# Optimization experiments

Measured on AMD Instinct MI355X. Metric: run time of the kernel, lower is better.

Reference implementation:

```python
import jax, jax.numpy as jnp
import numpy as np

B, N, K = 8, 2048, 16   # batch, points, neighbors (after dropping self)
EPS = 1e-5


def _bn(y, g, b, m, v):
    # eval-mode batchnorm over channel dim 1, y: [B,C,...]
    sh = (1, -1) + (1,) * (y.ndim - 2)
    inv = g.reshape(sh) / jnp.sqrt(v.reshape(sh) + EPS)
    return (y - m.reshape(sh)) * inv + b.reshape(sh)


def setup_inputs() -> dict:
    key = jax.random.key(0)
    ks = jax.random.split(key, 16)
    d = {}
    d["x"] = jax.random.normal(ks[0], (B, 3, N), dtype=jnp.float32)
    # pre: Conv1d(3->24, k=1) + BN
    d["w_pre"] = jax.random.normal(ks[1], (24, 3), dtype=jnp.float32) * 0.3
    d["b_pre"] = jax.random.normal(ks[2], (24,), dtype=jnp.float32) * 0.1
    d["g_pre"] = 1.0 + 0.1 * jax.random.normal(ks[3], (24,), dtype=jnp.float32)
    d["be_pre"] = 0.1 * jax.random.normal(ks[4], (24,), dtype=jnp.float32)
    d["m_pre"] = 0.1 * jax.random.normal(ks[5], (24,), dtype=jnp.float32)
    d["v_pre"] = jax.random.uniform(ks[6], (24,), minval=0.5, maxval=1.5, dtype=jnp.float32)
    # shared_mlp_1: Conv2d(48->12, 1, bias=False) + BN
    d["w1"] = jax.random.normal(ks[7], (12, 48), dtype=jnp.float32) * 0.15
    d["g1"] = 1.0 + 0.1 * jax.random.normal(ks[8], (12,), dtype=jnp.float32)
    d["be1"] = 0.1 * jax.random.normal(ks[9], (12,), dtype=jnp.float32)
    d["m1"] = 0.1 * jax.random.normal(ks[10], (12,), dtype=jnp.float32)
    d["v1"] = jax.random.uniform(ks[11], (12,), minval=0.5, maxval=1.5, dtype=jnp.float32)
    # shared_mlp_2: Conv2d(60->12, 1, bias=False) + BN
    d["w2"] = jax.random.normal(ks[12], (12, 60), dtype=jnp.float32) * 0.15
    d["g2"] = 1.0 + 0.1 * jax.random.normal(ks[13], (12,), dtype=jnp.float32)
    d["be2"] = 0.1 * jax.random.normal(ks[14], (12,), dtype=jnp.float32)
    d["m2"] = 0.1 * jax.random.normal(ks[15], (12,), dtype=jnp.float32)
    d["v2"] = jnp.ones((12,), dtype=jnp.float32)
    # shared_mlp_3: Conv2d(72->12, 1, bias=False), no BN
    d["w3"] = jax.random.normal(jax.random.fold_in(key, 99), (12, 72), dtype=jnp.float32) * 0.15
    return d


def reference(x, w_pre, b_pre, g_pre, be_pre, m_pre, v_pre,
              w1, g1, be1, m1, v1, w2, g2, be2, m2, v2, w3):
    # pre: 1x1 conv1d + BN + ReLU -> [B,24,N]
    pre = jnp.einsum('oc,bcn->bon', w_pre, x) + b_pre[None, :, None]
    pre = jax.nn.relu(_bn(pre, g_pre, be_pre, m_pre, v_pre))

    # kNN on xyz = x.detach(): [B,N,3]
    pts = jax.lax.stop_gradient(jnp.swapaxes(x, 1, 2))
    sq = jnp.sum(pts * pts, axis=-1)                              # [B,N]
    d2 = sq[:, :, None] + sq[:, None, :] - 2.0 * jnp.einsum('bnc,bmc->bnm', pts, pts)
    _, idx = jax.lax.top_k(-d2, K + 1)                             # nearest K+1 incl. self
    idx = idx[..., 1:]                                             # drop self -> [B,N,K]

    # gather neighbor features: [B,24,N,K]
    grouped = jax.vmap(lambda f, i: f[:, i])(pre, idx)
    center = jnp.broadcast_to(pre[..., None], grouped.shape)
    y = jnp.concatenate([center, grouped], axis=1)                 # [B,48,N,K]

    h1 = jax.nn.relu(_bn(jnp.einsum('oc,bcnk->bonk', w1, y), g1, be1, m1, v1))
    y = jnp.concatenate([h1, y], axis=1)                           # [B,60,N,K]
    h2 = jax.nn.relu(_bn(jnp.einsum('oc,bcnk->bonk', w2, y), g2, be2, m2, v2))
    y = jnp.concatenate([h2, y], axis=1)                           # [B,72,N,K]
    h3 = jnp.einsum('oc,bcnk->bonk', w3, y)
    y = jnp.concatenate([h3, y], axis=1)                           # [B,84,N,K]

    y = jnp.max(y, axis=-1)                                        # maxpool over neighbors -> [B,84,N]
    return jnp.concatenate([y, x], axis=1)                         # [B,87,N]
```

## Files before the change

kernel.cpp:

```cpp
#include <hip/hip_runtime.h>
#include <math.h>

#define EPS 1e-5f
#define NBATCH 8
#define NPTS 2048
#define KNB 16
#define BIG 3.2e38f

#define KNN_BLKS (NBATCH * 64)
#define FUSED_LDS 54400

#define WS_PRE 0
#define WS_AUX (16384 * 24)
#define WS_IDX (WS_AUX + 16384 * 72)

__device__ __forceinline__ float dist2f(float mex, float mey, float mez,
                                        float sqn, float4 q) {
  float dot2 = fmaf(mex, q.x, fmaf(mey, q.y, __fmul_rn(mez, q.z)));
  return __fsub_rn(__fadd_rn(sqn, q.w), dot2);
}

__global__ __launch_bounds__(512, 4) void fused_kernel(
    const float* __restrict__ x,
    const float* __restrict__ w_pre, const float* __restrict__ b_pre,
    const float* __restrict__ g_pre, const float* __restrict__ be_pre,
    const float* __restrict__ m_pre, const float* __restrict__ v_pre,
    const float* __restrict__ w1, const float* __restrict__ g1,
    const float* __restrict__ be1, const float* __restrict__ m1,
    const float* __restrict__ v1,
    const float* __restrict__ w2, const float* __restrict__ g2,
    const float* __restrict__ be2, const float* __restrict__ m2,
    const float* __restrict__ v2, const float* __restrict__ w3,
    float* __restrict__ pre, float* __restrict__ aux,
    int* __restrict__ knn_out) {
  extern __shared__ char smem[];
  float4* C4   = (float4*)smem;
  float* slist = (float*)(smem + 32768);
  float* fwp = (float*)(smem + 32768);
  float* fbp = fwp + 72;
  float* fw1 = fbp + 24;
  float* fb1 = fw1 + 576;
  float* fw2 = fb1 + 12;
  float* fb2 = fw2 + 720;
  float* sd2   = (float*)(smem + 49152);
  int*   sidx  = (int*)(smem + 51712);
  int*   scnt  = (int*)(smem + 54272);

  int tid = threadIdx.x;
  int bi = blockIdx.x;
  int b = bi >> 6, chunk = bi & 63;
  const float* xb = x + (size_t)b * 3 * NPTS;

  for (int j = tid; j < NPTS; j += 512) {
    float xx = xb[j], yy = xb[NPTS + j], zz = xb[2 * NPTS + j];
    float sq = __fadd_rn(__fadd_rn(__fmul_rn(xx, xx), __fmul_rn(yy, yy)),
                         __fmul_rn(zz, zz));
    C4[j] = make_float4(2.0f * xx, 2.0f * yy, 2.0f * zz, sq);
  }
  if (tid < 72) { int o = tid / 3; fwp[tid] = w_pre[tid] * (g_pre[o] / sqrtf(v_pre[o] + EPS)); }
  if (tid < 24) { float inv = g_pre[tid] / sqrtf(v_pre[tid] + EPS);
                  fbp[tid] = (b_pre[tid] - m_pre[tid]) * inv + be_pre[tid]; }
  for (int j = tid; j < 576; j += 512) { int o = j / 48; fw1[j] = w1[j] * (g1[o] / sqrtf(v1[o] + EPS)); }
  if (tid < 12) { float inv = g1[tid] / sqrtf(v1[tid] + EPS); fb1[tid] = be1[tid] - m1[tid] * inv; }
  for (int j = tid; j < 720; j += 512) { int o = j / 60; fw2[j] = w2[j] * (g2[o] / sqrtf(v2[o] + EPS)); }
  if (tid < 12) { float inv = g2[tid] / sqrtf(v2[tid] + EPS); fb2[tid] = be2[tid] - m2[tid] * inv; }
  for (int j = tid; j < 32 * 20; j += 512) sidx[j] = 0;
  if (tid < 32) scnt[tid] = 0;
  __syncthreads();

  {
    int r = tid & 15, pt = tid >> 4;
    int n0 = chunk * 32 + pt;
    size_t pgl = (size_t)(b << 11) + n0;
    float x0 = xb[n0], x1 = xb[NPTS + n0], x2 = xb[2 * NPTS + n0];
    float pr[24];
#pragma unroll
    for (int c = 0; c < 24; ++c) {
      float v = fmaf(fwp[c * 3 + 0], x0,
                fmaf(fwp[c * 3 + 1], x1,
                fmaf(fwp[c * 3 + 2], x2, fbp[c])));
      pr[c] = fmaxf(v, 0.f);
    }
    if (r == 0) {
      float4* o4 = (float4*)(pre + pgl * 24);
#pragma unroll
      for (int i = 0; i < 6; ++i)
        o4[i] = make_float4(pr[4*i], pr[4*i+1], pr[4*i+2], pr[4*i+3]);
    }
    if (r < 12) {
      int o = r;
      float u1 = fb1[o], a1 = 0.f, u2 = fb2[o], a2 = 0.f, u3 = 0.f, a3 = 0.f;
#pragma unroll
      for (int i = 0; i < 24; ++i) {
        u1 = fmaf(fw1[o*48 + i],      pr[i], u1);
        a1 = fmaf(fw1[o*48 + 24 + i], pr[i], a1);
        u2 = fmaf(fw2[o*60 + 12 + i], pr[i], u2);
        a2 = fmaf(fw2[o*60 + 36 + i], pr[i], a2);
        u3 = fmaf(w3[o*72 + 24 + i],  pr[i], u3);
        a3 = fmaf(w3[o*72 + 48 + i],  pr[i], a3);
      }
      float* A = aux + pgl * 72;
      A[o] = u1; A[12 + o] = u2; A[24 + o] = u3;
      A[36 + o] = a1; A[48 + o] = a2; A[60 + o] = a3;
    }
  }
  __syncthreads();

  int p = tid & 31, s = tid >> 5;
  int n = chunk * 32 + p;
  float4 me4 = C4[n];
  float mex = 0.5f * me4.x, mey = 0.5f * me4.y, mez = 0.5f * me4.z;
  float sqn = me4.w;
  const float4* Cs = C4 + s * 128;
  int selfc = n - s * 128;
  float L[16];
#pragma unroll
  for (int t = 0; t < 16; ++t) L[t] = BIG;
  for (int c0 = 0; c0 < 128; c0 += 16) {
    float S[16];
#pragma unroll
    for (int cc = 0; cc < 16; ++cc) {
      float4 q = Cs[c0 + cc];
      float d2 = dist2f(mex, mey, mez, sqn, q);
      S[cc] = ((c0 + cc) == selfc) ? BIG : d2;
    }
#pragma unroll
    for (int pw = 1; pw < 16; pw <<= 1) {
#pragma unroll
      for (int k = pw; k >= 1; k >>= 1) {
#pragma unroll
        for (int j = (k & (pw - 1)); j + k < 16; j += 2 * k) {
#pragma unroll
          for (int i = 0; i < k; ++i) {
            int a = i + j, bq = i + j + k;
            if (bq < 16 && (a / (2 * pw) == bq / (2 * pw))) {
              float lo = fminf(S[a], S[bq]);
              float hi = fmaxf(S[a], S[bq]);
              S[a] = lo; S[bq] = hi;
            }
          }
        }
      }
    }
    float m[16];
#pragma unroll
    for (int i = 0; i < 16; ++i) m[i] = fminf(L[i], S[15 - i]);
#pragma unroll
    for (int d = 8; d >= 1; d >>= 1) {
#pragma unroll
      for (int i = 0; i < 16; ++i) {
        if (!(i & d)) {
          float lo = fminf(m[i], m[i | d]);
          float hi = fmaxf(m[i], m[i | d]);
          m[i] = lo; m[i | d] = hi;
        }
      }
    }
#pragma unroll
    for (int i = 0; i < 16; ++i) L[i] = m[i];
  }
  {
    float bb[16], m16[16];
#pragma unroll
    for (int i = 0; i < 16; ++i) bb[i] = __shfl_xor(L[i], 32, 64);
#pragma unroll
    for (int i = 0; i < 16; ++i) m16[i] = fminf(L[i], bb[15 - i]);
#pragma unroll
    for (int d = 8; d >= 1; d >>= 1) {
#pragma unroll
      for (int i = 0; i < 16; ++i) {
        if (!(i & d)) {
          float lo = fminf(m16[i], m16[i | d]);
          float hi = fmaxf(m16[i], m16[i | d]);
          m16[i] = lo; m16[i | d] = hi;
        }
      }
    }
    if (!(s & 1)) {
#pragma unroll
      for (int i = 0; i < 16; ++i) slist[((s >> 1) * 16 + i) * 32 + p] = m16[i];
    }
  }
  __syncthreads();
  for (int W = 4; W >= 1; W >>= 1) {
    int w = tid >> 5;
    bool act = (w < W);
    float a[16], bb[16];
    if (act) {
#pragma unroll
      for (int i = 0; i < 16; ++i) a[i]  = slist[((2 * w) * 16 + i) * 32 + p];
#pragma unroll
      for (int i = 0; i < 16; ++i) bb[i] = slist[((2 * w + 1) * 16 + i) * 32 + p];
    }
    __syncthreads();
    if (act) {
      float m16[16];
#pragma unroll
      for (int i = 0; i < 16; ++i) m16[i] = fminf(a[i], bb[15 - i]);
#pragma unroll
      for (int d = 8; d >= 1; d >>= 1) {
#pragma unroll
        for (int i = 0; i < 16; ++i) {
          if (!(i & d)) {
            float lo = fminf(m16[i], m16[i | d]);
            float hi = fmaxf(m16[i], m16[i | d]);
            m16[i] = lo; m16[i | d] = hi;
          }
        }
      }
#pragma unroll
      for (int i = 0; i < 16; ++i) slist[(w * 16 + i) * 32 + p] = m16[i];
    }
    __syncthreads();
  }
  float tau = slist[15 * 32 + p];
#pragma unroll 4
  for (int c = 0; c < 128; ++c) {
    float4 q = Cs[c];
    float d2 = dist2f(mex, mey, mez, sqn, q);
    int j = s * 128 + c;
    if (d2 <= tau && j != n) {
      int pos = atomicAdd(&scnt[p], 1);
      if (pos < 20) { sd2[p * 20 + pos] = d2; sidx[p * 20 + pos] = j; }
    }
  }
  __syncthreads();
  if (tid < 32) {
    int c = scnt[tid]; if (c > 20) c = 20;
    if (c > 16) {
      for (int t = 0; t < 16; ++t) {
        int best = t;
        for (int u = t + 1; u < c; ++u) {
          float da = sd2[tid * 20 + u], db = sd2[tid * 20 + best];
          int ia = sidx[tid * 20 + u], ib = sidx[tid * 20 + best];
          if (da < db || (da == db && ia < ib)) best = u;
        }
        float td = sd2[tid * 20 + t]; sd2[tid * 20 + t] = sd2[tid * 20 + best]; sd2[tid * 20 + best] = td;
        int ti = sidx[tid * 20 + t]; sidx[tid * 20 + t] = sidx[tid * 20 + best]; sidx[tid * 20 + best] = ti;
      }
    }
  }
  __syncthreads();
  {
    int pp = tid >> 4, kk = tid & 15;
    knn_out[((size_t)b * NPTS + chunk * 32 + pp) * KNB + kk] = sidx[pp * 20 + kk];
  }
}

__global__ __launch_bounds__(256) void mlp_kernel(
    const float* __restrict__ pre, const float* __restrict__ aux,
    const int* __restrict__ knn, const float* __restrict__ x,
    const float* __restrict__ w2, const float* __restrict__ g2,
    const float* __restrict__ v2, const float* __restrict__ w3,
    float* __restrict__ out) {
  __shared__ float sW2h[144], sW3h2[144], sW3h1[144];
  __shared__ float sout[87 * 16];
  int tid = threadIdx.x;
  if (tid < 144) {
    int o = tid / 12, i = tid - o * 12;
    float inv2 = g2[o] / sqrtf(v2[o] + EPS);
    sW2h[tid]  = w2[o * 60 + i] * inv2;
    sW3h2[tid] = w3[o * 72 + i];
    sW3h1[tid] = w3[o * 72 + 12 + i];
  }
  __syncthreads();
  int k = tid & 15, pl = tid >> 4;
  int p = blockIdx.x * 16 + pl;
  int b = p >> 11, n = p & (NPTS - 1);
  int nb = knn[(size_t)p * KNB + k];
  const float4* u4 = (const float4*)(aux + (size_t)p * 72);
  const float4* a4 = (const float4*)(aux + ((size_t)(b << 11) + nb) * 72 + 36);
  float uc[36], av[36];
#pragma unroll
  for (int i = 0; i < 9; ++i) {
    float4 t = u4[i];
    uc[4*i] = t.x; uc[4*i+1] = t.y; uc[4*i+2] = t.z; uc[4*i+3] = t.w;
    float4 t2 = a4[i];
    av[4*i] = t2.x; av[4*i+1] = t2.y; av[4*i+2] = t2.z; av[4*i+3] = t2.w;
  }
  float h1[12], h2[12], h3[12];
#pragma unroll
  for (int o = 0; o < 12; ++o) h1[o] = fmaxf(uc[o] + av[o], 0.f);
#pragma unroll
  for (int o = 0; o < 12; ++o) {
    float a = uc[12 + o] + av[12 + o];
#pragma unroll
    for (int i = 0; i < 12; ++i) a = fmaf(sW2h[o * 12 + i], h1[i], a);
    h2[o] = fmaxf(a, 0.f);
  }
#pragma unroll
  for (int o = 0; o < 12; ++o) {
    float a = uc[24 + o] + av[24 + o];
#pragma unroll
    for (int i = 0; i < 12; ++i) a = fmaf(sW3h2[o * 12 + i], h2[i], a);
#pragma unroll
    for (int i = 0; i < 12; ++i) a = fmaf(sW3h1[o * 12 + i], h1[i], a);
    h3[o] = a;
  }
  float nbf[24];
  const float4* pn4 = (const float4*)(pre + ((size_t)(b << 11) + nb) * 24);
#pragma unroll
  for (int i = 0; i < 6; ++i) {
    float4 t = pn4[i];
    nbf[4*i] = t.x; nbf[4*i+1] = t.y; nbf[4*i+2] = t.z; nbf[4*i+3] = t.w;
  }
#pragma unroll
  for (int m = 1; m < 16; m <<= 1) {
#pragma unroll
    for (int o = 0; o < 12; ++o) {
      h1[o] = fmaxf(h1[o], __shfl_xor(h1[o], m, 16));
      h2[o] = fmaxf(h2[o], __shfl_xor(h2[o], m, 16));
      h3[o] = fmaxf(h3[o], __shfl_xor(h3[o], m, 16));
    }
#pragma unroll
    for (int i = 0; i < 24; ++i)
      nbf[i] = fmaxf(nbf[i], __shfl_xor(nbf[i], m, 16));
  }
  if (k == 0) {
    const float4* c4 = (const float4*)(pre + (size_t)p * 24);
#pragma unroll
    for (int o = 0; o < 12; ++o) {
      sout[(0  + o) * 16 + pl] = h3[o];
      sout[(12 + o) * 16 + pl] = h2[o];
      sout[(24 + o) * 16 + pl] = h1[o];
    }
#pragma unroll
    for (int i = 0; i < 6; ++i) {
      float4 t = c4[i];
      sout[(36 + 4*i    ) * 16 + pl] = t.x;
      sout[(36 + 4*i + 1) * 16 + pl] = t.y;
      sout[(36 + 4*i + 2) * 16 + pl] = t.z;
      sout[(36 + 4*i + 3) * 16 + pl] = t.w;
    }
#pragma unroll
    for (int i = 0; i < 24; ++i) sout[(60 + i) * 16 + pl] = nbf[i];
    const float* xb = x + (size_t)b * 3 * NPTS + n;
    sout[84 * 16 + pl] = xb[0];
    sout[85 * 16 + pl] = xb[NPTS];
    sout[86 * 16 + pl] = xb[2 * NPTS];
  }
  __syncthreads();
  int n0 = (blockIdx.x * 16) & (NPTS - 1);
  float* ob = out + (size_t)b * 87 * NPTS;
  for (int j2 = tid; j2 < 87 * 16; j2 += 256) {
    int c = j2 >> 4, i = j2 & 15;
    ob[(size_t)c * NPTS + n0 + i] = sout[j2];
  }
}

extern "C" void kernel_launch(void* const* d_in, const int* in_sizes, int n_in,
                              void* d_out, int out_size, void* d_ws, size_t ws_size,
                              hipStream_t stream) {
  (void)in_sizes; (void)n_in; (void)out_size; (void)ws_size;
  const float* x     = (const float*)d_in[0];
  const float* w_pre = (const float*)d_in[1];
  const float* b_pre = (const float*)d_in[2];
  const float* g_pre = (const float*)d_in[3];
  const float* be_pre= (const float*)d_in[4];
  const float* m_pre = (const float*)d_in[5];
  const float* v_pre = (const float*)d_in[6];
  const float* w1    = (const float*)d_in[7];
  const float* g1    = (const float*)d_in[8];
  const float* be1   = (const float*)d_in[9];
  const float* m1    = (const float*)d_in[10];
  const float* v1    = (const float*)d_in[11];
  const float* w2    = (const float*)d_in[12];
  const float* g2    = (const float*)d_in[13];
  const float* be2   = (const float*)d_in[14];
  const float* m2    = (const float*)d_in[15];
  const float* v2    = (const float*)d_in[16];
  const float* w3    = (const float*)d_in[17];
  float* ws  = (float*)d_ws;
  float* pre = ws + WS_PRE;
  float* aux = ws + WS_AUX;
  int*   knn = (int*)(ws + WS_IDX);
  float* out = (float*)d_out;

  fused_kernel<<<KNN_BLKS, 512, FUSED_LDS, stream>>>(
      x, w_pre, b_pre, g_pre, be_pre, m_pre, v_pre,
      w1, g1, be1, m1, v1, w2, g2, be2, m2, v2, w3,
      pre, aux, knn);
  mlp_kernel<<<NBATCH * NPTS / 16, 256, 0, stream>>>(pre, aux, knn, x,
                                                     w2, g2, v2, w3, out);
}
```

Before: 156.0 us.

## Halve points per KNN block, double blocks, shrink LDS and transpose weights

Each fused block now handles 16 query points instead of 32. That doubles the grid to 1024 blocks, and each thread scans 64 candidates instead of 128. The extra partial top-16 merge is done with a second wave shuffle, and LDS is reorganized and reduced so more blocks can be resident (launch bounds now allow 8). The folded MLP weights are stored transposed in LDS so lanes read consecutive addresses, and w3 is staged in LDS. The trade-off is that every block still loads all 2048 points into LDS, so the redundant staging work doubles, and the extra sync and merge steps add overhead.

```diff
diff --git a/kernel.cpp b/kernel.cpp
--- a/kernel.cpp
+++ b/kernel.cpp
@@ -7,8 +7,9 @@
 #define KNB 16
 #define BIG 3.2e38f
 
-#define KNN_BLKS (NBATCH * 64)
-#define FUSED_LDS 54400
+#define CHUNK_PTS 16
+#define KNN_BLKS (NBATCH * 128)
+#define FUSED_LDS 40960
 
 #define WS_PRE 0
 #define WS_AUX (16384 * 24)
@@ -20,7 +21,7 @@
   return __fsub_rn(__fadd_rn(sqn, q.w), dot2);
 }
 
-__global__ __launch_bounds__(512, 4) void fused_kernel(
+__global__ __launch_bounds__(512, 8) void fused_kernel(
     const float* __restrict__ x,
     const float* __restrict__ w_pre, const float* __restrict__ b_pre,
     const float* __restrict__ g_pre, const float* __restrict__ be_pre,
@@ -36,19 +37,23 @@
   extern __shared__ char smem[];
   float4* C4   = (float4*)smem;
   float* slist = (float*)(smem + 32768);
-  float* fwp = (float*)(smem + 32768);
-  float* fbp = fwp + 72;
-  float* fw1 = fbp + 24;
-  float* fb1 = fw1 + 576;
-  float* fw2 = fb1 + 12;
-  float* fb2 = fw2 + 720;
-  float* sd2   = (float*)(smem + 49152);
-  int*   sidx  = (int*)(smem + 51712);
-  int*   scnt  = (int*)(smem + 54272);
+  float* fwp   = slist;
+  float* fbp   = fwp + 72;
+  float* fw1t  = fbp + 24;
+  float* fb1   = fw1t + 576;
+  float* fw2t  = fb1 + 12;
+  float* fb2   = fw2t + 720;
+  float* fw3t  = fb2 + 12;
+  float* sinv1 = fw3t + 576;
+  float* sinv2 = sinv1 + 12;
+  float* sinvP = sinv2 + 12;
+  float* sd2  = slist;
+  int*   sidx = (int*)(slist + 320);
+  int*   scnt = (int*)(slist + 640);
 
   int tid = threadIdx.x;
   int bi = blockIdx.x;
-  int b = bi >> 6, chunk = bi & 63;
+  int b = bi >> 7, chunk = bi & 127;
   const float* xb = x + (size_t)b * 3 * NPTS;
 
   for (int j = tid; j < NPTS; j += 512) {
@@ -57,20 +62,22 @@
                          __fmul_rn(zz, zz));
     C4[j] = make_float4(2.0f * xx, 2.0f * yy, 2.0f * zz, sq);
   }
-  if (tid < 72) { int o = tid / 3; fwp[tid] = w_pre[tid] * (g_pre[o] / sqrtf(v_pre[o] + EPS)); }
-  if (tid < 24) { float inv = g_pre[tid] / sqrtf(v_pre[tid] + EPS);
-                  fbp[tid] = (b_pre[tid] - m_pre[tid]) * inv + be_pre[tid]; }
-  for (int j = tid; j < 576; j += 512) { int o = j / 48; fw1[j] = w1[j] * (g1[o] / sqrtf(v1[o] + EPS)); }
-  if (tid < 12) { float inv = g1[tid] / sqrtf(v1[tid] + EPS); fb1[tid] = be1[tid] - m1[tid] * inv; }
-  for (int j = tid; j < 720; j += 512) { int o = j / 60; fw2[j] = w2[j] * (g2[o] / sqrtf(v2[o] + EPS)); }
-  if (tid < 12) { float inv = g2[tid] / sqrtf(v2[tid] + EPS); fb2[tid] = be2[tid] - m2[tid] * inv; }
-  for (int j = tid; j < 32 * 20; j += 512) sidx[j] = 0;
-  if (tid < 32) scnt[tid] = 0;
+  if (tid < 24) sinvP[tid] = g_pre[tid] / sqrtf(v_pre[tid] + EPS);
+  if (tid < 12) { sinv1[tid] = g1[tid] / sqrtf(v1[tid] + EPS);
+                  sinv2[tid] = g2[tid] / sqrtf(v2[tid] + EPS); }
+  __syncthreads();
+  if (tid < 72) fwp[tid] = w_pre[tid] * sinvP[tid / 3];
+  if (tid < 24) fbp[tid] = (b_pre[tid] - m_pre[tid]) * sinvP[tid] + be_pre[tid];
+  if (tid < 12) { fb1[tid] = be1[tid] - m1[tid] * sinv1[tid];
+                  fb2[tid] = be2[tid] - m2[tid] * sinv2[tid]; }
+  for (int j = tid; j < 576; j += 512) { int i = j / 12, o = j - i * 12; fw1t[j] = w1[o * 48 + i] * sinv1[o]; }
+  for (int j = tid; j < 720; j += 512) { int i = j / 12, o = j - i * 12; fw2t[j] = w2[o * 60 + i] * sinv2[o]; }
+  for (int j = tid; j < 576; j += 512) { int i = j / 12, o = j - i * 12; fw3t[j] = w3[o * 72 + 24 + i]; }
   __syncthreads();
 
   {
-    int r = tid & 15, pt = tid >> 4;
-    int n0 = chunk * 32 + pt;
+    int rr = tid & 31, pt = tid >> 5;
+    int n0 = chunk * CHUNK_PTS + pt;
     size_t pgl = (size_t)(b << 11) + n0;
     float x0 = xb[n0], x1 = xb[NPTS + n0], x2 = xb[2 * NPTS + n0];
     float pr[24];
@@ -81,23 +88,23 @@
                 fmaf(fwp[c * 3 + 2], x2, fbp[c])));
       pr[c] = fmaxf(v, 0.f);
     }
-    if (r == 0) {
+    if (rr == 16) {
       float4* o4 = (float4*)(pre + pgl * 24);
 #pragma unroll
       for (int i = 0; i < 6; ++i)
         o4[i] = make_float4(pr[4*i], pr[4*i+1], pr[4*i+2], pr[4*i+3]);
     }
-    if (r < 12) {
-      int o = r;
+    if (rr < 12) {
+      int o = rr;
       float u1 = fb1[o], a1 = 0.f, u2 = fb2[o], a2 = 0.f, u3 = 0.f, a3 = 0.f;
 #pragma unroll
       for (int i = 0; i < 24; ++i) {
-        u1 = fmaf(fw1[o*48 + i],      pr[i], u1);
-        a1 = fmaf(fw1[o*48 + 24 + i], pr[i], a1);
-        u2 = fmaf(fw2[o*60 + 12 + i], pr[i], u2);
-        a2 = fmaf(fw2[o*60 + 36 + i], pr[i], a2);
-        u3 = fmaf(w3[o*72 + 24 + i],  pr[i], u3);
-        a3 = fmaf(w3[o*72 + 48 + i],  pr[i], a3);
+        u1 = fmaf(fw1t[i * 12 + o],        pr[i], u1);
+        a1 = fmaf(fw1t[(24 + i) * 12 + o], pr[i], a1);
+        u2 = fmaf(fw2t[(12 + i) * 12 + o], pr[i], u2);
+        a2 = fmaf(fw2t[(36 + i) * 12 + o], pr[i], a2);
+        u3 = fmaf(fw3t[i * 12 + o],        pr[i], u3);
+        a3 = fmaf(fw3t[(24 + i) * 12 + o], pr[i], a3);
       }
       float* A = aux + pgl * 72;
       A[o] = u1; A[12 + o] = u2; A[24 + o] = u3;
@@ -106,17 +113,17 @@
   }
   __syncthreads();
 
-  int p = tid & 31, s = tid >> 5;
-  int n = chunk * 32 + p;
+  int p = tid & 15, s = tid >> 4;
+  int n = chunk * CHUNK_PTS + p;
   float4 me4 = C4[n];
   float mex = 0.5f * me4.x, mey = 0.5f * me4.y, mez = 0.5f * me4.z;
   float sqn = me4.w;
-  const float4* Cs = C4 + s * 128;
-  int selfc = n - s * 128;
+  const float4* Cs = C4 + s * 64;
+  int selfc = n - s * 64;
   float L[16];
 #pragma unroll
   for (int t = 0; t < 16; ++t) L[t] = BIG;
-  for (int c0 = 0; c0 < 128; c0 += 16) {
+  for (int c0 = 0; c0 < 64; c0 += 16) {
     float S[16];
 #pragma unroll
     for (int cc = 0; cc < 16; ++cc) {
@@ -162,7 +169,7 @@
   {
     float bb[16], m16[16];
 #pragma unroll
-    for (int i = 0; i < 16; ++i) bb[i] = __shfl_xor(L[i], 32, 64);
+    for (int i = 0; i < 16; ++i) bb[i] = __shfl_xor(L[i], 16, 64);
 #pragma unroll
     for (int i = 0; i < 16; ++i) m16[i] = fminf(L[i], bb[15 - i]);
 #pragma unroll
@@ -176,21 +183,37 @@
         }
       }
     }
-    if (!(s & 1)) {
-#pragma unroll
-      for (int i = 0; i < 16; ++i) slist[((s >> 1) * 16 + i) * 32 + p] = m16[i];
+#pragma unroll
+    for (int i = 0; i < 16; ++i) bb[i] = __shfl_xor(m16[i], 32, 64);
+    float m2_[16];
+#pragma unroll
+    for (int i = 0; i < 16; ++i) m2_[i] = fminf(m16[i], bb[15 - i]);
+#pragma unroll
+    for (int d = 8; d >= 1; d >>= 1) {
+#pragma unroll
+      for (int i = 0; i < 16; ++i) {
+        if (!(i & d)) {
+          float lo = fminf(m2_[i], m2_[i | d]);
+          float hi = fmaxf(m2_[i], m2_[i | d]);
+          m2_[i] = lo; m2_[i | d] = hi;
+        }
+      }
+    }
+    if ((s & 3) == 0) {
+#pragma unroll
+      for (int i = 0; i < 16; ++i) slist[((s >> 2) * 16 + i) * 16 + p] = m2_[i];
     }
   }
   __syncthreads();
   for (int W = 4; W >= 1; W >>= 1) {
-    int w = tid >> 5;
+    int w = tid >> 4;
     bool act = (w < W);
     float a[16], bb[16];
     if (act) {
 #pragma unroll
-      for (int i = 0; i < 16; ++i) a[i]  = slist[((2 * w) * 16 + i) * 32 + p];
-#pragma unroll
-      for (int i = 0; i < 16; ++i) bb[i] = slist[((2 * w + 1) * 16 + i) * 32 + p];
+      for (int i = 0; i < 16; ++i) a[i]  = slist[((2 * w) * 16 + i) * 16 + p];
+#pragma unroll
+      for (int i = 0; i < 16; ++i) bb[i] = slist[((2 * w + 1) * 16 + i) * 16 + p];
     }
     __syncthreads();
     if (act) {
@@ -209,23 +232,27 @@
         }
       }
 #pragma unroll
-      for (int i = 0; i < 16; ++i) slist[(w * 16 + i) * 32 + p] = m16[i];
+      for (int i = 0; i < 16; ++i) slist[(w * 16 + i) * 16 + p] = m16[i];
     }
     __syncthreads();
   }
-  float tau = slist[15 * 32 + p];
+  float tau = slist[15 * 16 + p];
+  __syncthreads();
+  for (int j = tid; j < 16 * 20; j += 512) sidx[j] = 0;
+  if (tid < 16) scnt[tid] = 0;
+  __syncthreads();
 #pragma unroll 4
-  for (int c = 0; c < 128; ++c) {
+  for (int c = 0; c < 64; ++c) {
     float4 q = Cs[c];
     float d2 = dist2f(mex, mey, mez, sqn, q);
-    int j = s * 128 + c;
+    int j = s * 64 + c;
     if (d2 <= tau && j != n) {
       int pos = atomicAdd(&scnt[p], 1);
       if (pos < 20) { sd2[p * 20 + pos] = d2; sidx[p * 20 + pos] = j; }
     }
   }
   __syncthreads();
-  if (tid < 32) {
+  if (tid < 16) {
     int c = scnt[tid]; if (c > 20) c = 20;
     if (c > 16) {
       for (int t = 0; t < 16; ++t) {
@@ -241,9 +268,9 @@
     }
   }
   __syncthreads();
-  {
+  if (tid < 256) {
     int pp = tid >> 4, kk = tid & 15;
-    knn_out[((size_t)b * NPTS + chunk * 32 + pp) * KNB + kk] = sidx[pp * 20 + kk];
+    knn_out[((size_t)b * NPTS + chunk * CHUNK_PTS + pp) * KNB + kk] = sidx[pp * 20 + kk];
   }
 }
 
```

Result: no change. 155.7 us (-0.2%).
